# Performance work log

Hardware: AMD Instinct MI355X
Metric: run time of the kernel (lower is better)

## Reference

```python
import jax, jax.numpy as jnp
import numpy as np

EMB = 1024
HEADS = 16
HEAD_DIM = EMB // HEADS  # 64


def setup_inputs() -> dict:
    key = jax.random.key(0)
    ks = jax.random.split(key, 11)
    B, S = 2, 2048
    scale = 1.0 / np.sqrt(EMB)
    inp = {
        "xv": jax.random.normal(ks[0], (B, S, EMB), jnp.float32),
        "xk": jax.random.normal(ks[1], (B, S, EMB), jnp.float32),
        "xq": jax.random.normal(ks[2], (B, S, EMB), jnp.float32),
        "Wq": jax.random.normal(ks[3], (EMB, EMB), jnp.float32) * scale,
        "bq": jax.random.normal(ks[4], (EMB,), jnp.float32) * 0.01,
        "Wk": jax.random.normal(ks[5], (EMB, EMB), jnp.float32) * scale,
        "bk": jax.random.normal(ks[6], (EMB,), jnp.float32) * 0.01,
        "Wv": jax.random.normal(ks[7], (EMB, EMB), jnp.float32) * scale,
        "bv": jax.random.normal(ks[8], (EMB,), jnp.float32) * 0.01,
        "Wo": jax.random.normal(ks[9], (EMB, EMB), jnp.float32) * scale,
        "bo": jax.random.normal(ks[10], (EMB,), jnp.float32) * 0.01,
    }
    return inp


def reference(xv, xk, xq, Wq, bq, Wk, bk, Wv, bv, Wo, bo):
    B, S, E = xq.shape
    H, D = HEADS, HEAD_DIM
    # projections (x @ W + b), split into heads: [B,S,H,D]
    Q = (xq @ Wq + bq).reshape(B, S, H, D)
    K = (xk @ Wk + bk).reshape(B, S, H, D)
    V = (xv @ Wv + bv).reshape(B, S, H, D)
    # scaled dot-product attention per head (vectorized over heads)
    scores = jnp.einsum("bqhd,bkhd->bhqk", Q, K) / jnp.sqrt(jnp.float32(D))
    attn = jax.nn.softmax(scores, axis=-1)
    ctx = jnp.einsum("bhqk,bkhd->bqhd", attn, V).reshape(B, S, E)
    return ctx @ Wo + bo
```

## Files before the change

### kernel.cpp

```cpp
#include <hip/hip_runtime.h>
#include <hip/hip_bf16.h>

typedef __hip_bfloat16 bf16;
typedef __attribute__((ext_vector_type(8))) short short8;
typedef __attribute__((ext_vector_type(4))) short short4v;
typedef __attribute__((ext_vector_type(4))) float floatx4;

#define MFMA16 __builtin_amdgcn_mfma_f32_16x16x32_bf16
#define BARRIER __builtin_amdgcn_s_barrier
#define SCHEDB0() __builtin_amdgcn_sched_barrier(0)


__device__ __forceinline__ void gl16(const void* g, void* l) {
    __builtin_amdgcn_global_load_lds(
        (const __attribute__((address_space(1))) void*)g,
        (__attribute__((address_space(3))) void*)l, 16, 0, 0);
}

__global__ __launch_bounds__(256) void wtrans_k(const float* __restrict__ w0,
                                                const float* __restrict__ w1,
                                                const float* __restrict__ w2,
                                                const float* __restrict__ w3,
                                                bf16* __restrict__ dst) {
    const float* srcs[4] = {w0, w1, w2, w3};
    const float* src = srcs[blockIdx.z];
    bf16* d = dst + (size_t)blockIdx.z * 1024 * 1024;
    __shared__ float t[32][33];
    int tx = threadIdx.x, ty = threadIdx.y;
    int x0 = blockIdx.x * 32, y0 = blockIdx.y * 32;
#pragma unroll
    for (int i = 0; i < 4; i++)
        t[ty + i * 8][tx] = src[(size_t)(y0 + ty + i * 8) * 1024 + x0 + tx];
    __syncthreads();
#pragma unroll
    for (int i = 0; i < 4; i++)
        d[(size_t)(x0 + ty + i * 8) * 1024 + y0 + tx] =
            __float2bfloat16(t[tx][ty + i * 8]);
}

__global__ __launch_bounds__(256) void xcast_k(const float* __restrict__ x0,
                                               const float* __restrict__ x1,
                                               const float* __restrict__ x2,
                                               bf16* __restrict__ dst) {
    const float* srcs[3] = {x0, x1, x2};
    const float* src = srcs[blockIdx.y];
    bf16* d = dst + (size_t)blockIdx.y * (4096 * 1024);
    size_t i = (size_t)blockIdx.x * 256 + threadIdx.x;
    const float4* s4 = (const float4*)src + i * 2;
    float4 a = s4[0], b = s4[1];
    union { __hip_bfloat162 h2[4]; short8 s; } pk;
    pk.h2[0] = __float22bfloat162_rn(make_float2(a.x, a.y));
    pk.h2[1] = __float22bfloat162_rn(make_float2(a.z, a.w));
    pk.h2[2] = __float22bfloat162_rn(make_float2(b.x, b.y));
    pk.h2[3] = __float22bfloat162_rn(make_float2(b.z, b.w));
    *(short8*)&d[i * 8] = pk.s;
}

__global__ __launch_bounds__(256) void qkv_k(const bf16* __restrict__ xb,
                                             const bf16* __restrict__ wt,
                                             const float* __restrict__ bq,
                                             const float* __restrict__ bk,
                                             const float* __restrict__ bv,
                                             bf16* __restrict__ Qw,
                                             bf16* __restrict__ Kw,
                                             bf16* __restrict__ Vt) {
    __shared__ __align__(16) bf16 lA[2][128 * 32];
    __shared__ __align__(16) bf16 lB[2][128 * 32];
    int z = blockIdx.z;
    const bf16* A = xb + (size_t)z * (4096 * 1024);
    const bf16* Bt = wt + (size_t)z * (1024 * 1024);
    const float* bias = (z == 0) ? bq : (z == 1) ? bk : bv;
    int m0 = blockIdx.x * 128, n0 = blockIdx.y * 128;
    int tid = threadIdx.x, wave = tid >> 6, lane = tid & 63;
    int lm = lane & 15, quad = lane >> 4;
    int wm = wave >> 1, wn = wave & 1;
    int swb = quad ^ ((lm >> 1) & 3);

    floatx4 acc[4][4];
#pragma unroll
    for (int i = 0; i < 4; i++)
#pragma unroll
        for (int j = 0; j < 4; j++) acc[i][j] = (floatx4){0.f, 0.f, 0.f, 0.f};

    auto stage = [&](int bufi, int kt) {
#pragma unroll
        for (int q2 = 0; q2 < 2; q2++) {
            int slot0 = wave * 128 + q2 * 64;
            int r = (slot0 + lane) >> 2;
            int c = (lane & 3) ^ ((r >> 1) & 3);
            gl16(&A[(size_t)(m0 + r) * 1024 + kt * 32 + c * 8],
                 &lA[bufi][slot0 * 8]);
            gl16(&Bt[(size_t)(n0 + r) * 1024 + kt * 32 + c * 8],
                 &lB[bufi][slot0 * 8]);
        }
    };

    auto compute = [&](int cur) {
        short8 af[4], bfr[4];
#pragma unroll
        for (int ms = 0; ms < 4; ms++) {
            int r = wm * 64 + ms * 16 + lm;
            af[ms] = *(const short8*)&lA[cur][(r * 4 + swb) * 8];
        }
#pragma unroll
        for (int ns = 0; ns < 4; ns++) {
            int r = wn * 64 + ns * 16 + lm;
            bfr[ns] = *(const short8*)&lB[cur][(r * 4 + swb) * 8];
        }
#pragma unroll
        for (int ms = 0; ms < 4; ms++)
#pragma unroll
            for (int ns = 0; ns < 4; ns++)
                acc[ms][ns] = MFMA16(af[ms], bfr[ns], acc[ms][ns], 0, 0, 0);
    };

    stage(0, 0);
    for (int kt = 0; kt < 31; kt++) {
        int cur = kt & 1;
        BARRIER();
        stage(cur ^ 1, kt + 1);
        asm volatile("s_waitcnt vmcnt(4)" ::: "memory");
        BARRIER();
        SCHEDB0();
        compute(cur);
    }
    BARRIER();
    asm volatile("s_waitcnt vmcnt(0)" ::: "memory");
    BARRIER();
    SCHEDB0();
    compute(1);

    bf16* dstQK = (z == 0) ? Qw : Kw;
    float scale = (z == 0) ? 0.125f * 1.44269504f : 1.0f;
#pragma unroll
    for (int ms = 0; ms < 4; ms++) {
        int rowb = m0 + wm * 64 + ms * 16 + quad * 4;
        int bb = rowb >> 11, s0 = rowb & 2047;
#pragma unroll
        for (int ns = 0; ns < 4; ns++) {
            int col = n0 + wn * 64 + ns * 16 + lm;
            float bvv = bias[col];
            int hh = col >> 6, d = col & 63;
            if (z < 2) {
#pragma unroll
                for (int rr = 0; rr < 4; rr++) {
                    float v = (acc[ms][ns][rr] + bvv) * scale;
                    dstQK[((((size_t)bb * 16 + hh) * 2048 + s0 + rr) << 6) + d] =
                        __float2bfloat16(v);
                }
            } else {
                short4v pk;
#pragma unroll
                for (int rr = 0; rr < 4; rr++) {
                    bf16 h = __float2bfloat16(acc[ms][ns][rr] + bvv);
                    pk[rr] = *(short*)&h;
                }
                *(short4v*)&Vt[((((size_t)bb * 16 + hh) * 64 + d) << 11) + s0] = pk;
            }
        }
    }
}

__global__ __launch_bounds__(256) void outproj_k(const bf16* __restrict__ ctx,
                                                 const bf16* __restrict__ wot,
                                                 const float* __restrict__ bo,
                                                 float* __restrict__ out) {
    __shared__ __align__(16) bf16 lA[2][128 * 32];
    __shared__ __align__(16) bf16 lB[2][64 * 32];
    int m0 = blockIdx.x * 128, n0 = blockIdx.y * 64;
    int tid = threadIdx.x, wave = tid >> 6, lane = tid & 63;
    int lm = lane & 15, quad = lane >> 4;
    int wm = wave >> 1, wn = wave & 1;
    int swb = quad ^ ((lm >> 1) & 3);

    floatx4 acc[4][2];
#pragma unroll
    for (int i = 0; i < 4; i++)
#pragma unroll
        for (int j = 0; j < 2; j++) acc[i][j] = (floatx4){0.f, 0.f, 0.f, 0.f};

    auto stage = [&](int bufi, int kt) {
#pragma unroll
        for (int q2 = 0; q2 < 2; q2++) {
            int slot0 = wave * 128 + q2 * 64;
            int r = (slot0 + lane) >> 2;
            int c = (lane & 3) ^ ((r >> 1) & 3);
            gl16(&ctx[(size_t)(m0 + r) * 1024 + kt * 32 + c * 8],
                 &lA[bufi][slot0 * 8]);
        }
        {
            int slot0 = wave * 64;
            int r = (slot0 + lane) >> 2;
            int c = (lane & 3) ^ ((r >> 1) & 3);
            gl16(&wot[(size_t)(n0 + r) * 1024 + kt * 32 + c * 8],
                 &lB[bufi][slot0 * 8]);
        }
    };

    auto compute = [&](int cur) {
        short8 af[4], bfr[2];
#pragma unroll
        for (int ms = 0; ms < 4; ms++) {
            int r = wm * 64 + ms * 16 + lm;
            af[ms] = *(const short8*)&lA[cur][(r * 4 + swb) * 8];
        }
#pragma unroll
        for (int ns = 0; ns < 2; ns++) {
            int r = wn * 32 + ns * 16 + lm;
            bfr[ns] = *(const short8*)&lB[cur][(r * 4 + swb) * 8];
        }
#pragma unroll
        for (int ms = 0; ms < 4; ms++)
#pragma unroll
            for (int ns = 0; ns < 2; ns++)
                acc[ms][ns] = MFMA16(af[ms], bfr[ns], acc[ms][ns], 0, 0, 0);
    };

    stage(0, 0);
    for (int kt = 0; kt < 31; kt++) {
        int cur = kt & 1;
        BARRIER();
        stage(cur ^ 1, kt + 1);
        asm volatile("s_waitcnt vmcnt(3)" ::: "memory");
        BARRIER();
        SCHEDB0();
        compute(cur);
    }
    BARRIER();
    asm volatile("s_waitcnt vmcnt(0)" ::: "memory");
    BARRIER();
    SCHEDB0();
    compute(1);

#pragma unroll
    for (int ms = 0; ms < 4; ms++) {
        int rowb = m0 + wm * 64 + ms * 16 + quad * 4;
#pragma unroll
        for (int ns = 0; ns < 2; ns++) {
            int col = n0 + wn * 32 + ns * 16 + lm;
            float bvv = bo[col];
#pragma unroll
            for (int rr = 0; rr < 4; rr++)
                out[(size_t)(rowb + rr) * 1024 + col] = acc[ms][ns][rr] + bvv;
        }
    }
}

__global__ __launch_bounds__(256) void attn_k(const bf16* __restrict__ Q,
                                              const bf16* __restrict__ K,
                                              const bf16* __restrict__ Vt,
                                              bf16* __restrict__ ctx) {
    __shared__ __align__(16) bf16 lK[2][64 * 64];
    __shared__ __align__(16) bf16 lV[2][64 * 64];
    __shared__ __align__(16) bf16 lP[64 * 64];
    int bh = blockIdx.x, qt = blockIdx.y;
    int b = bh >> 4, h = bh & 15;
    const bf16* Qh = Q + (size_t)bh * (2048 * 64);
    const bf16* Kh = K + (size_t)bh * (2048 * 64);
    const bf16* Vh = Vt + (size_t)bh * (64 * 2048);
    int tid = threadIdx.x, wave = tid >> 6, lane = tid & 63;
    int lm = lane & 15, quad = lane >> 4;
    int s7 = lm & 7;

    int qrow = qt * 64 + wave * 16 + lm;
    short8 qf0 = *(const short8*)&Qh[(size_t)qrow * 64 + quad * 8];
    short8 qf1 = *(const short8*)&Qh[(size_t)qrow * 64 + 32 + quad * 8];

    short8 onesf;
#pragma unroll
    for (int i = 0; i < 8; i++) onesf[i] = (short)0x3F80;

    floatx4 o[4];
#pragma unroll
    for (int i = 0; i < 4; i++) o[i] = (floatx4){0.f, 0.f, 0.f, 0.f};
    floatx4 accL = (floatx4){0.f, 0.f, 0.f, 0.f};

    auto stage = [&](int bufi, int kt) {
#pragma unroll
        for (int q2 = 0; q2 < 2; q2++) {
            int slot0 = wave * 128 + q2 * 64;
            int r = (slot0 + lane) >> 3;
            int c = (lane & 7) ^ (r & 7);
            gl16(&Kh[(size_t)(kt * 64 + r) * 64 + c * 8], &lK[bufi][slot0 * 8]);
            gl16(&Vh[(size_t)r * 2048 + kt * 64 + c * 8], &lV[bufi][slot0 * 8]);
        }
    };

    char* lProw = (char*)lP + (wave * 16 + lm) * 128;

    auto compute = [&](int cur) {
        floatx4 s[4];
#pragma unroll
        for (int i = 0; i < 4; i++) s[i] = (floatx4){0.f, 0.f, 0.f, 0.f};
#pragma unroll
        for (int ns = 0; ns < 4; ns++) {
            int r = ns * 16 + lm;
            short8 kf0 = *(const short8*)&lK[cur][(r * 8 + (quad ^ s7)) * 8];
            short8 kf1 = *(const short8*)&lK[cur][(r * 8 + ((4 + quad) ^ s7)) * 8];
            s[ns] = MFMA16(kf0, qf0, s[ns], 0, 0, 0);
            s[ns] = MFMA16(kf1, qf1, s[ns], 0, 0, 0);
        }

#pragma unroll
        for (int ns = 0; ns < 4; ns++) {
            float p0 = __builtin_amdgcn_exp2f(s[ns][0]);
            float p1 = __builtin_amdgcn_exp2f(s[ns][1]);
            float p2 = __builtin_amdgcn_exp2f(s[ns][2]);
            float p3 = __builtin_amdgcn_exp2f(s[ns][3]);
            union { __hip_bfloat162 h2[2]; short4v s4; } pk;
            pk.h2[0] = __float22bfloat162_rn(make_float2(p0, p1));
            pk.h2[1] = __float22bfloat162_rn(make_float2(p2, p3));
            int sw = (2 * ns + (quad >> 1)) ^ s7;
            *(short4v*)(lProw + sw * 16 + (quad & 1) * 8) = pk.s4;
        }

#pragma unroll
        for (int kk = 0; kk < 2; kk++) {
            int c2 = (kk * 4 + quad) ^ s7;
            short8 pf = *(const short8*)(lProw + c2 * 16);
            accL = MFMA16(pf, onesf, accL, 0, 0, 0);
#pragma unroll
            for (int ns = 0; ns < 4; ns++) {
                int r = ns * 16 + lm;
                short8 vf = *(const short8*)&lV[cur][(r * 8 + ((kk * 4 + quad) ^ s7)) * 8];
                o[ns] = MFMA16(pf, vf, o[ns], 0, 0, 0);
            }
        }
    };

    stage(0, 0);
    for (int kt = 0; kt < 31; kt++) {
        int cur = kt & 1;
        BARRIER();
        stage(cur ^ 1, kt + 1);
        asm volatile("s_waitcnt vmcnt(4)" ::: "memory");
        BARRIER();
        SCHEDB0();
        compute(cur);
    }
    BARRIER();
    asm volatile("s_waitcnt vmcnt(0)" ::: "memory");
    BARRIER();
    SCHEDB0();
    compute(1);

    float inv[4];
#pragma unroll
    for (int rr = 0; rr < 4; rr++) inv[rr] = 1.f / accL[rr];

#pragma unroll
    for (int ns = 0; ns < 4; ns++) {
        int e = h * 64 + ns * 16 + lm;
#pragma unroll
        for (int rr = 0; rr < 4; rr++) {
            int srow = qt * 64 + wave * 16 + quad * 4 + rr;
            ctx[(size_t)(b * 2048 + srow) * 1024 + e] =
                __float2bfloat16(o[ns][rr] * inv[rr]);
        }
    }
}

extern "C" void kernel_launch(void* const* d_in, const int* in_sizes, int n_in,
                              void* d_out, int out_size, void* d_ws, size_t ws_size,
                              hipStream_t stream) {
    const float* xv = (const float*)d_in[0];
    const float* xk = (const float*)d_in[1];
    const float* xq = (const float*)d_in[2];
    const float* Wq = (const float*)d_in[3];
    const float* bq = (const float*)d_in[4];
    const float* Wk = (const float*)d_in[5];
    const float* bk = (const float*)d_in[6];
    const float* Wv = (const float*)d_in[7];
    const float* bv = (const float*)d_in[8];
    const float* Wo = (const float*)d_in[9];
    const float* bo = (const float*)d_in[10];
    float* out = (float*)d_out;
    bf16* ws = (bf16*)d_ws;

    const size_t MB1 = 1024 * 1024;
    bf16* wt  = ws;
    bf16* Qw  = ws + 4 * MB1;
    bf16* Kw  = ws + 8 * MB1;
    bf16* Vt  = ws + 12 * MB1;
    bf16* ctx = ws + 16 * MB1;
    bf16* xb  = ws + 20 * MB1;

    hipLaunchKernelGGL(wtrans_k, dim3(32, 32, 4), dim3(32, 8), 0, stream,
                       Wq, Wk, Wv, Wo, wt);

    hipLaunchKernelGGL(xcast_k, dim3(2048, 3), dim3(256), 0, stream,
                       xq, xk, xv, xb);

    hipLaunchKernelGGL(qkv_k, dim3(32, 8, 3), dim3(256), 0, stream,
                       xb, wt, bq, bk, bv, Qw, Kw, Vt);

    hipLaunchKernelGGL(attn_k, dim3(32, 32), dim3(256), 0, stream, Qw, Kw, Vt, ctx);

    hipLaunchKernelGGL(outproj_k, dim3(32, 16), dim3(256), 0, stream,
                       ctx, wt + 3 * MB1, bo, out);
}
```

Before: 228.1 us.

## Double attention query tile per block, triple-buffer QKV GEMM, add MFMA priority hints

The attention kernel now processes 128 query rows per block (32 per wave, two 16-row subtiles). Each K/V tile loaded into LDS is reused across twice as many queries, and the grid shrinks by half. The QKV projection GEMM switches from double to triple buffering with a deeper prefetch distance to hide global-load latency. s_setprio is raised around MFMA clusters in all three GEMM-style kernels. The costs are more registers and LDS per block, which may lower occupancy, and fewer attention blocks to fill the CUs.

Measured after the change: 219.3 us. -3.9%, faster.

```diff
diff --git a/kernel.cpp b/kernel.cpp
--- a/kernel.cpp
+++ b/kernel.cpp
@@ -9,6 +9,7 @@
 #define MFMA16 __builtin_amdgcn_mfma_f32_16x16x32_bf16
 #define BARRIER __builtin_amdgcn_s_barrier
 #define SCHEDB0() __builtin_amdgcn_sched_barrier(0)
+#define SETPRIO __builtin_amdgcn_s_setprio
 
 
 __device__ __forceinline__ void gl16(const void* g, void* l) {
@@ -64,8 +65,8 @@
                                              bf16* __restrict__ Qw,
                                              bf16* __restrict__ Kw,
                                              bf16* __restrict__ Vt) {
-    __shared__ __align__(16) bf16 lA[2][128 * 32];
-    __shared__ __align__(16) bf16 lB[2][128 * 32];
+    __shared__ __align__(16) bf16 lA[3][128 * 32];
+    __shared__ __align__(16) bf16 lB[3][128 * 32];
     int z = blockIdx.z;
     const bf16* A = xb + (size_t)z * (4096 * 1024);
     const bf16* Bt = wt + (size_t)z * (1024 * 1024);
@@ -107,28 +108,32 @@
             int r = wn * 64 + ns * 16 + lm;
             bfr[ns] = *(const short8*)&lB[cur][(r * 4 + swb) * 8];
         }
+        SETPRIO(1);
 #pragma unroll
         for (int ms = 0; ms < 4; ms++)
 #pragma unroll
             for (int ns = 0; ns < 4; ns++)
                 acc[ms][ns] = MFMA16(af[ms], bfr[ns], acc[ms][ns], 0, 0, 0);
+        SETPRIO(0);
     };
 
     stage(0, 0);
-    for (int kt = 0; kt < 31; kt++) {
-        int cur = kt & 1;
-        BARRIER();
-        stage(cur ^ 1, kt + 1);
-        asm volatile("s_waitcnt vmcnt(4)" ::: "memory");
+    stage(1, 1);
+    for (int kt = 0; kt < 32; kt++) {
+        int cur = kt % 3;
+        BARRIER();
+        if (kt < 30) {
+            stage((kt + 2) % 3, kt + 2);
+            asm volatile("s_waitcnt vmcnt(8)" ::: "memory");
+        } else if (kt == 30) {
+            asm volatile("s_waitcnt vmcnt(4)" ::: "memory");
+        } else {
+            asm volatile("s_waitcnt vmcnt(0)" ::: "memory");
+        }
         BARRIER();
         SCHEDB0();
         compute(cur);
     }
-    BARRIER();
-    asm volatile("s_waitcnt vmcnt(0)" ::: "memory");
-    BARRIER();
-    SCHEDB0();
-    compute(1);
 
     bf16* dstQK = (z == 0) ? Qw : Kw;
     float scale = (z == 0) ? 0.125f * 1.44269504f : 1.0f;
@@ -209,11 +214,13 @@
             int r = wn * 32 + ns * 16 + lm;
             bfr[ns] = *(const short8*)&lB[cur][(r * 4 + swb) * 8];
         }
+        SETPRIO(1);
 #pragma unroll
         for (int ms = 0; ms < 4; ms++)
 #pragma unroll
             for (int ns = 0; ns < 2; ns++)
                 acc[ms][ns] = MFMA16(af[ms], bfr[ns], acc[ms][ns], 0, 0, 0);
+        SETPRIO(0);
     };
 
     stage(0, 0);
@@ -252,7 +259,7 @@
                                               bf16* __restrict__ ctx) {
     __shared__ __align__(16) bf16 lK[2][64 * 64];
     __shared__ __align__(16) bf16 lV[2][64 * 64];
-    __shared__ __align__(16) bf16 lP[64 * 64];
+    __shared__ __align__(16) bf16 lP[128 * 64];
     int bh = blockIdx.x, qt = blockIdx.y;
     int b = bh >> 4, h = bh & 15;
     const bf16* Qh = Q + (size_t)bh * (2048 * 64);
@@ -262,18 +269,25 @@
     int lm = lane & 15, quad = lane >> 4;
     int s7 = lm & 7;
 
-    int qrow = qt * 64 + wave * 16 + lm;
-    short8 qf0 = *(const short8*)&Qh[(size_t)qrow * 64 + quad * 8];
-    short8 qf1 = *(const short8*)&Qh[(size_t)qrow * 64 + 32 + quad * 8];
+    short8 qf[2][2];
+#pragma unroll
+    for (int qh = 0; qh < 2; qh++) {
+        int qrow = qt * 128 + wave * 32 + qh * 16 + lm;
+        qf[qh][0] = *(const short8*)&Qh[(size_t)qrow * 64 + quad * 8];
+        qf[qh][1] = *(const short8*)&Qh[(size_t)qrow * 64 + 32 + quad * 8];
+    }
 
     short8 onesf;
 #pragma unroll
     for (int i = 0; i < 8; i++) onesf[i] = (short)0x3F80;
 
-    floatx4 o[4];
-#pragma unroll
-    for (int i = 0; i < 4; i++) o[i] = (floatx4){0.f, 0.f, 0.f, 0.f};
-    floatx4 accL = (floatx4){0.f, 0.f, 0.f, 0.f};
+    floatx4 o[2][4];
+#pragma unroll
+    for (int qh = 0; qh < 2; qh++)
+#pragma unroll
+        for (int i = 0; i < 4; i++) o[qh][i] = (floatx4){0.f, 0.f, 0.f, 0.f};
+    floatx4 accL[2] = {(floatx4){0.f, 0.f, 0.f, 0.f},
+                       (floatx4){0.f, 0.f, 0.f, 0.f}};
 
     auto stage = [&](int bufi, int kt) {
 #pragma unroll
@@ -286,46 +300,62 @@
         }
     };
 
-    char* lProw = (char*)lP + (wave * 16 + lm) * 128;
+    char* lPr0 = (char*)lP + (wave * 32 + lm) * 128;
+    char* lPr1 = lPr0 + 16 * 128;
 
     auto compute = [&](int cur) {
-        floatx4 s[4];
-#pragma unroll
-        for (int i = 0; i < 4; i++) s[i] = (floatx4){0.f, 0.f, 0.f, 0.f};
+        floatx4 s[2][4];
+#pragma unroll
+        for (int qh = 0; qh < 2; qh++)
+#pragma unroll
+            for (int i = 0; i < 4; i++) s[qh][i] = (floatx4){0.f, 0.f, 0.f, 0.f};
+        SETPRIO(1);
 #pragma unroll
         for (int ns = 0; ns < 4; ns++) {
             int r = ns * 16 + lm;
             short8 kf0 = *(const short8*)&lK[cur][(r * 8 + (quad ^ s7)) * 8];
             short8 kf1 = *(const short8*)&lK[cur][(r * 8 + ((4 + quad) ^ s7)) * 8];
-            s[ns] = MFMA16(kf0, qf0, s[ns], 0, 0, 0);
-            s[ns] = MFMA16(kf1, qf1, s[ns], 0, 0, 0);
-        }
-
-#pragma unroll
-        for (int ns = 0; ns < 4; ns++) {
-            float p0 = __builtin_amdgcn_exp2f(s[ns][0]);
-            float p1 = __builtin_amdgcn_exp2f(s[ns][1]);
-            float p2 = __builtin_amdgcn_exp2f(s[ns][2]);
-            float p3 = __builtin_amdgcn_exp2f(s[ns][3]);
-            union { __hip_bfloat162 h2[2]; short4v s4; } pk;
-            pk.h2[0] = __float22bfloat162_rn(make_float2(p0, p1));
-            pk.h2[1] = __float22bfloat162_rn(make_float2(p2, p3));
-            int sw = (2 * ns + (quad >> 1)) ^ s7;
-            *(short4v*)(lProw + sw * 16 + (quad & 1) * 8) = pk.s4;
-        }
-
+            s[0][ns] = MFMA16(kf0, qf[0][0], s[0][ns], 0, 0, 0);
+            s[0][ns] = MFMA16(kf1, qf[0][1], s[0][ns], 0, 0, 0);
+            s[1][ns] = MFMA16(kf0, qf[1][0], s[1][ns], 0, 0, 0);
+            s[1][ns] = MFMA16(kf1, qf[1][1], s[1][ns], 0, 0, 0);
+        }
+        SETPRIO(0);
+
+#pragma unroll
+        for (int qh = 0; qh < 2; qh++) {
+            char* pr = qh ? lPr1 : lPr0;
+#pragma unroll
+            for (int ns = 0; ns < 4; ns++) {
+                float p0 = __builtin_amdgcn_exp2f(s[qh][ns][0]);
+                float p1 = __builtin_amdgcn_exp2f(s[qh][ns][1]);
+                float p2 = __builtin_amdgcn_exp2f(s[qh][ns][2]);
+                float p3 = __builtin_amdgcn_exp2f(s[qh][ns][3]);
+                union { __hip_bfloat162 h2[2]; short4v s4; } pk;
+                pk.h2[0] = __float22bfloat162_rn(make_float2(p0, p1));
+                pk.h2[1] = __float22bfloat162_rn(make_float2(p2, p3));
+                int sw = (2 * ns + (quad >> 1)) ^ s7;
+                *(short4v*)(pr + sw * 16 + (quad & 1) * 8) = pk.s4;
+            }
+        }
+
+        SETPRIO(1);
 #pragma unroll
         for (int kk = 0; kk < 2; kk++) {
             int c2 = (kk * 4 + quad) ^ s7;
-            short8 pf = *(const short8*)(lProw + c2 * 16);
-            accL = MFMA16(pf, onesf, accL, 0, 0, 0);
+            short8 pf0 = *(const short8*)(lPr0 + c2 * 16);
+            short8 pf1 = *(const short8*)(lPr1 + c2 * 16);
+            accL[0] = MFMA16(pf0, onesf, accL[0], 0, 0, 0);
+            accL[1] = MFMA16(pf1, onesf, accL[1], 0, 0, 0);
 #pragma unroll
             for (int ns = 0; ns < 4; ns++) {
                 int r = ns * 16 + lm;
                 short8 vf = *(const short8*)&lV[cur][(r * 8 + ((kk * 4 + quad) ^ s7)) * 8];
-                o[ns] = MFMA16(pf, vf, o[ns], 0, 0, 0);
+                o[0][ns] = MFMA16(pf0, vf, o[0][ns], 0, 0, 0);
+                o[1][ns] = MFMA16(pf1, vf, o[1][ns], 0, 0, 0);
             }
         }
+        SETPRIO(0);
     };
 
     stage(0, 0);
@@ -344,18 +374,23 @@
     SCHEDB0();
     compute(1);
 
-    float inv[4];
-#pragma unroll
-    for (int rr = 0; rr < 4; rr++) inv[rr] = 1.f / accL[rr];
-
-#pragma unroll
-    for (int ns = 0; ns < 4; ns++) {
-        int e = h * 64 + ns * 16 + lm;
-#pragma unroll
-        for (int rr = 0; rr < 4; rr++) {
-            int srow = qt * 64 + wave * 16 + quad * 4 + rr;
-            ctx[(size_t)(b * 2048 + srow) * 1024 + e] =
-                __float2bfloat16(o[ns][rr] * inv[rr]);
+    float inv[2][4];
+#pragma unroll
+    for (int qh = 0; qh < 2; qh++)
+#pragma unroll
+        for (int rr = 0; rr < 4; rr++) inv[qh][rr] = 1.f / accL[qh][rr];
+
+#pragma unroll
+    for (int qh = 0; qh < 2; qh++) {
+#pragma unroll
+        for (int ns = 0; ns < 4; ns++) {
+            int e = h * 64 + ns * 16 + lm;
+#pragma unroll
+            for (int rr = 0; rr < 4; rr++) {
+                int srow = qt * 128 + wave * 32 + qh * 16 + quad * 4 + rr;
+                ctx[(size_t)(b * 2048 + srow) * 1024 + e] =
+                    __float2bfloat16(o[qh][ns][rr] * inv[qh][rr]);
+            }
         }
     }
 }
@@ -394,7 +429,7 @@
     hipLaunchKernelGGL(qkv_k, dim3(32, 8, 3), dim3(256), 0, stream,
                        xb, wt, bq, bk, bv, Qw, Kw, Vt);
 
-    hipLaunchKernelGGL(attn_k, dim3(32, 32), dim3(256), 0, stream, Qw, Kw, Vt, ctx);
+    hipLaunchKernelGGL(attn_k, dim3(32, 16), dim3(256), 0, stream, Qw, Kw, Vt, ctx);
 
     hipLaunchKernelGGL(outproj_k, dim3(32, 16), dim3(256), 0, stream,
                        ctx, wt + 3 * MB1, bo, out);
```
